# Kernel optimization log

Hardware: AMD Instinct MI355X
Metric: run time of the kernel (lower is better)

Reference implementation:

```python
import jax, jax.numpy as jnp
import numpy as np

HID = 128      # hidden_features
NF = 32        # noise_features
NPL = NF // 4  # noise features per layer
RES = 512      # noise grid resolution
N = 262144     # number of query points


def leaky_relu(x):
    return jax.nn.leaky_relu(x, negative_slope=0.01)


def sample_bilinear(image, coords):
    """image: [M, H, W]; coords: [..., M, 2] -> [..., M]"""
    M, Hn, Wn = image.shape
    x = coords[..., 0] - 0.5
    y = coords[..., 1] - 0.5
    x0f = jnp.floor(x)
    y0f = jnp.floor(y)
    xw = x - x0f
    yw = y - y0f
    x0 = x0f.astype(jnp.int32) % Wn
    x1 = (x0f.astype(jnp.int32) + 1) % Wn
    y0 = y0f.astype(jnp.int32) % Hn
    y1 = (y0f.astype(jnp.int32) + 1) % Hn
    f = jnp.arange(M)  # broadcasts against [..., M] index arrays
    i00 = image[f, y0, x0]
    i01 = image[f, y0, x1]
    i10 = image[f, y1, x0]
    i11 = image[f, y1, x1]
    i0 = i00 + (i01 - i00) * xw
    i1 = i10 + (i11 - i10) * xw
    return i0 + (i1 - i0) * yw


def setup_inputs() -> dict:
    key = jax.random.key(0)
    ks = jax.random.split(key, 12)
    noise = jax.random.normal(ks[0], (NF, RES, RES), dtype=jnp.float32)
    coords = jax.random.normal(ks[1], (N, 2), dtype=jnp.float32)
    # NoiseTransforms param: randn * 0.05 * 2**i per feature
    scale = 0.05 * (2.0 ** np.arange(NF)).astype(np.float32)
    transformations = jax.random.normal(ks[2], (NF, 2, 2), dtype=jnp.float32) * scale[:, None, None]
    input_vec = jnp.ones((HID,), dtype=jnp.float32)
    s_lin = 1.0 / np.sqrt(HID)
    s_noise = 1.0 / np.sqrt(NPL)
    lw = jax.random.uniform(ks[3], (4, HID, HID), jnp.float32, -s_lin, s_lin)
    lb = jax.random.uniform(ks[4], (4, HID), jnp.float32, -s_lin, s_lin)
    lnw = jax.random.uniform(ks[5], (4, HID, NPL), jnp.float32, -s_noise, s_noise)
    tw1 = jax.random.uniform(ks[6], (HID, HID), jnp.float32, -s_lin, s_lin)
    tb1 = jax.random.uniform(ks[7], (HID,), jnp.float32, -s_lin, s_lin)
    tw2 = jax.random.uniform(ks[8], (1, HID), jnp.float32, -s_lin, s_lin)
    tb2 = jax.random.uniform(ks[9], (1,), jnp.float32, -s_lin, s_lin)
    return {"noise": noise, "coords": coords, "transformations": transformations,
            "input_vec": input_vec, "lw": lw, "lb": lb, "lnw": lnw,
            "tw1": tw1, "tb1": tb1, "tw2": tw2, "tb2": tb2}


def reference(noise, coords, transformations, input_vec, lw, lb, lnw, tw1, tb1, tw2, tb2):
    # noise coords: [..., NF, 2]
    noise_coords = jnp.einsum('...n,Mmn->...Mm', coords, transformations)
    noise_values = sample_bilinear(noise, noise_coords)  # [..., NF]
    x = input_vec  # [HID], broadcasts up through layer adds
    for i in range(4):
        nv = noise_values[..., i * NPL:(i + 1) * NPL]
        x = leaky_relu(jnp.einsum('...h,oh->...o', x, lw[i]) + lb[i]
                       + jnp.einsum('...n,on->...o', nv, lnw[i]))
    h = leaky_relu(jnp.einsum('...h,oh->...o', x, tw1) + tb1)
    return jnp.einsum('...h,oh->...o', h, tw2) + tb2  # [..., 1]
```

## Files before the change

kernel.cpp:

```cpp
#include <hip/hip_runtime.h>

typedef _Float16 f16;
typedef f16 f16x4 __attribute__((ext_vector_type(4)));
typedef f16 f16x8 __attribute__((ext_vector_type(8)));
typedef float f32x4 __attribute__((ext_vector_type(4)));

#define RES 512
#define PTS 128
#define XS  136
#define AS  16


__device__ __forceinline__
void pack_w_body(int g, const float* __restrict__ lw, const float* __restrict__ lnw,
                 const float* __restrict__ lb, const float* __restrict__ tw1,
                 const float* __restrict__ tb1, const float* __restrict__ ivec,
                 f16* __restrict__ wf, f16* __restrict__ waugf) {
    if (g < 10240) {
        const int L = g >> 11, r = g & 2047;
        const int lane = r & 63, frag = r >> 6;
        const int q = lane >> 4, l15 = lane & 15;
        const int mt = frag >> 2, c = frag & 3;
        const float* src = ((L < 4) ? (lw + L * 16384) : tw1)
                           + (mt * 16 + l15) * 128 + c * 32 + q * 8;
        f16x8 h;
        #pragma unroll
        for (int j = 0; j < 8; ++j) h[j] = (f16)src[j];
        *(f16x8*)(wf + (size_t)g * 8) = h;
    } else {
        const int ga = g - 10240;
        const int L = ga >> 9, r = ga & 511;
        const int lane = r & 63, mt = r >> 6;
        const int q = lane >> 4, l15 = lane & 15;
        const int row = mt * 16 + l15;
        f16x8 h = {};
        if (q == 0 && L < 4) {
            const float* src = lnw + L * 1024 + row * 8;
            #pragma unroll
            for (int j = 0; j < 8; ++j) h[j] = (f16)src[j];
        }
        if (q == 1) {
            if (L == 0) {
                float s = lb[row];
                const float4* w4 = (const float4*)(lw + row * 128);
                const float4* v4 = (const float4*)ivec;
                #pragma unroll 8
                for (int k = 0; k < 32; ++k) {
                    const float4 w = w4[k], v = v4[k];
                    s += w.x * v.x + w.y * v.y + w.z * v.z + w.w * v.w;
                }
                h[0] = (f16)s;
            } else {
                h[0] = (f16)((L < 4) ? lb[L * 128 + row] : tb1[row]);
            }
        }
        *(f16x8*)(waugf + (size_t)ga * 8) = h;
    }
}

__global__ __launch_bounds__(256)
void pack_all_k(const float* __restrict__ n, f16* __restrict__ q,
                const float* __restrict__ lw,  const float* __restrict__ lnw,
                const float* __restrict__ lb,  const float* __restrict__ tw1,
                const float* __restrict__ tb1, const float* __restrict__ ivec,
                f16* __restrict__ wf, f16* __restrict__ waugf) {
    const int b = blockIdx.x;
    if (b < 8192) {
        const int idx = b * 256 + threadIdx.x;
        const int qx = idx & 255, rest = idx >> 8;
        const int qy = rest & 255, m = rest >> 8;
        const float* src = n + ((size_t)m * 512 + 2 * qy) * 512 + 2 * qx;
        const float2 r0 = *(const float2*)(src);
        const float2 r1 = *(const float2*)(src + 512);
        f16x4 o; o[0]=(f16)r0.x; o[1]=(f16)r0.y; o[2]=(f16)r1.x; o[3]=(f16)r1.y;
        *(f16x4*)(q + (size_t)idx * 4) = o;
    } else {
        pack_w_body((b - 8192) * 256 + threadIdx.x, lw, lnw, lb, tw1, tb1, ivec, wf, waugf);
    }
}

__global__ __launch_bounds__(256)
void pack_w_k(const float* __restrict__ lw,  const float* __restrict__ lnw,
              const float* __restrict__ lb,  const float* __restrict__ tw1,
              const float* __restrict__ tb1, const float* __restrict__ ivec,
              f16* __restrict__ wf, f16* __restrict__ waugf) {
    pack_w_body(blockIdx.x * 256 + threadIdx.x, lw, lnw, lb, tw1, tb1, ivec, wf, waugf);
}

__device__ __forceinline__ float quad_tap(uint2 q, int sy, int sx) {
    unsigned w = sy ? q.y : q.x;
    w >>= (sx << 4);
    union { unsigned short u; f16 h; } cv; cv.u = (unsigned short)w;
    return (float)cv.h;
}

template <bool QUAD>
__global__ __launch_bounds__(256, 4)
void sample_kernel(const void* __restrict__ noise_v,
                   const float* __restrict__ coords,
                   const float* __restrict__ trans,
                   f16* __restrict__ nv_ws, const int Ntot)
{
    __shared__ float T_sh[128];
    const int t = threadIdx.x;
    if (t < 128) T_sh[t] = trans[t];
    __syncthreads();

    const int g = blockIdx.x & 7;
    const int pb = (blockIdx.x >> 3) * 1024 + t;

    int mk[4];
    if (g < 7) { mk[0] = g; mk[1] = g + 9; mk[2] = g + 17; mk[3] = g + 25; }
    else       { mk[0] = 7; mk[1] = 8;     mk[2] = 16;     mk[3] = 24;     }

    float2 c[4];
    #pragma unroll
    for (int j = 0; j < 4; ++j)
        c[j] = *(const float2*)(coords + (pb + 256 * j) * 2);

    float nvr[4][4];
    {
        #pragma clang fp contract(off)
        #pragma unroll
        for (int j = 0; j < 4; ++j) {
            const float cx = c[j].x;
            const float cy = c[j].y;
            #pragma unroll
            for (int k = 0; k < 4; ++k) {
                const int m = mk[k];
                const float T00 = T_sh[m*4+0], T01 = T_sh[m*4+1];
                const float T10 = T_sh[m*4+2], T11 = T_sh[m*4+3];
                const float p0x = T00 * cx;
                const float p0y = T10 * cx;
                const float ncx = __builtin_fmaf(T01, cy, p0x);
                const float ncy = __builtin_fmaf(T11, cy, p0y);
                const float u = ncx - 0.5f;
                const float v = ncy - 0.5f;
                const float xf = floorf(u), yf = floorf(v);
                const float xw = u - xf, yw = v - yf;
                int ix = (xf >= 2147483648.0f || xf < -2147483648.0f) ? (int)(-2147483647 - 1) : (int)xf;
                int iy = (yf >= 2147483648.0f || yf < -2147483648.0f) ? (int)(-2147483647 - 1) : (int)yf;
                const int x0 = ix & (RES - 1);
                const int x1 = (int)(((unsigned)ix + 1u) & (unsigned)(RES - 1));
                const int y0 = iy & (RES - 1);
                const int y1 = (int)(((unsigned)iy + 1u) & (unsigned)(RES - 1));
                float i00, i01, i10, i11;
                if constexpr (QUAD) {
                    const f16* pl = (const f16*)noise_v + (size_t)m * (256 * 256 * 4);
                    const int qx0 = x0 >> 1, sx0 = x0 & 1;
                    const int qx1 = x1 >> 1, sx1 = x1 & 1;
                    const int qy0 = y0 >> 1, sy0 = y0 & 1;
                    const int qy1 = y1 >> 1, sy1 = y1 & 1;
                    const uint2 qa = *(const uint2*)(pl + (qy0 * 256 + qx0) * 4);
                    const uint2 qb = *(const uint2*)(pl + (qy0 * 256 + qx1) * 4);
                    const uint2 qc = *(const uint2*)(pl + (qy1 * 256 + qx0) * 4);
                    const uint2 qd = *(const uint2*)(pl + (qy1 * 256 + qx1) * 4);
                    i00 = quad_tap(qa, sy0, sx0);
                    i01 = quad_tap(qb, sy0, sx1);
                    i10 = quad_tap(qc, sy1, sx0);
                    i11 = quad_tap(qd, sy1, sx1);
                } else {
                    const float* pl = (const float*)noise_v + (size_t)m * (RES * RES);
                    i00 = pl[y0 * RES + x0];
                    i01 = pl[y0 * RES + x1];
                    i10 = pl[y1 * RES + x0];
                    i11 = pl[y1 * RES + x1];
                }
                const float a0 = i00 + (i01 - i00) * xw;
                const float a1 = i10 + (i11 - i10) * xw;
                nvr[j][k] = a0 + (a1 - a0) * yw;
            }
        }
    }
    #pragma unroll
    for (int j = 0; j < 4; ++j) {
        #pragma unroll
        for (int k = 0; k < 4; ++k) {
            const int m = mk[k];
            const int slot = (m & 7) * 4 + (m >> 3);
            nv_ws[(size_t)slot * Ntot + pb + 256 * j] = (f16)nvr[j][k];
        }
    }
}

__global__ __launch_bounds__(256, 2)
void mlp_kernel(const f16* __restrict__ nv_ws,
                const f16* __restrict__ wf,
                const f16* __restrict__ waugf,
                const float* __restrict__ tw2,
                const float* __restrict__ tb2,
                float* __restrict__ out, const int Ntot)
{
    __shared__ f16 Wm[16384];
    __shared__ f16 Waug[4096];
    __shared__ f16 xa[PTS * XS];
    __shared__ f16 xaug[PTS * AS];
    __shared__ __align__(16) float tw2_sh[128];

    const int t    = threadIdx.x;
    const int wave = t >> 6;
    const int lane = t & 63;
    const int q    = lane >> 4;
    const int l15  = lane & 15;
    const int pbase = blockIdx.x * PTS;
    const int pw    = wave * 32;
    const int p = t >> 1, h = t & 1;

    if (t < 128) {
        tw2_sh[t] = tw2[t];
        xaug[t * AS + 8] = (f16)1.0f;
        #pragma unroll
        for (int c = 9; c < 16; ++c) xaug[t * AS + c] = (f16)0.0f;
    }
    const float tb2_0 = tb2[0];

    f16x8 nva, nvb;
    {
        const int P = pbase + p;
        #pragma unroll
        for (int j = 0; j < 8; ++j) {
            nva[j] = nv_ws[(size_t)(j * 4 + 2 * h)     * Ntot + P];
            nvb[j] = nv_ws[(size_t)(j * 4 + 2 * h + 1) * Ntot + P];
        }
    }
    if (h == 0) *(f16x8*)&xaug[p * AS] = nva;

    {
        const f16x8 a0 = *(const f16x8*)&waugf[t * 8];
        const f16x8 a1 = *(const f16x8*)&waugf[(t + 256) * 8];
        *(f16x8*)&Waug[t * 8]         = a0;
        *(f16x8*)&Waug[(t + 256) * 8] = a1;
    }
    __syncthreads();

    const f32x4 z4 = {0.f, 0.f, 0.f, 0.f};
    f32x4 acc[2][8];
    f16x8 wreg[8], areg[2];
    #pragma unroll 1
    for (int L = 0; L < 5; ++L) {
        if (L < 4) {
            const f16* wsrc = wf + (L + 1) * 16384;
            #pragma unroll
            for (int i = 0; i < 8; ++i)
                wreg[i] = *(const f16x8*)&wsrc[(t + i * 256) * 8];
            const f16* asrc = waugf + (L + 1) * 4096;
            areg[0] = *(const f16x8*)&asrc[t * 8];
            areg[1] = *(const f16x8*)&asrc[(t + 256) * 8];
        }

        if (L == 0) {
            #pragma unroll
            for (int i = 0; i < 2; ++i)
                #pragma unroll
                for (int mt = 0; mt < 8; ++mt) acc[i][mt] = z4;
        }
        const int pr0 = (pw + l15) * XS, pr1 = (pw + 16 + l15) * XS;
        if (L) {
            #pragma unroll
            for (int c = 0; c < 4; ++c) {
                const int kc = c * 32 + q * 8;
                const f16x8 xb0 = *(const f16x8*)&xa[pr0 + kc];
                const f16x8 xb1 = *(const f16x8*)&xa[pr1 + kc];
                #pragma unroll
                for (int mt = 0; mt < 8; ++mt) {
                    const f16x8 aw = *(const f16x8*)&Wm[((mt * 4 + c) * 64 + lane) * 8];
                    const f32x4 c0 = (c == 0) ? z4 : acc[0][mt];
                    const f32x4 c1 = (c == 0) ? z4 : acc[1][mt];
                    acc[0][mt] = __builtin_amdgcn_mfma_f32_16x16x32_f16(aw, xb0, c0, 0, 0, 0);
                    acc[1][mt] = __builtin_amdgcn_mfma_f32_16x16x32_f16(aw, xb1, c1, 0, 0, 0);
                }
            }
        }
        {
            f16x8 xb0 = {}, xb1 = {};
            if (q < 2) {
                xb0 = *(const f16x8*)&xaug[(pw + l15) * AS + q * 8];
                xb1 = *(const f16x8*)&xaug[(pw + 16 + l15) * AS + q * 8];
            }
            #pragma unroll
            for (int mt = 0; mt < 8; ++mt) {
                const f16x8 aw = *(const f16x8*)&Waug[(mt * 64 + lane) * 8];
                acc[0][mt] = __builtin_amdgcn_mfma_f32_16x16x32_f16(aw, xb0, acc[0][mt], 0, 0, 0);
                acc[1][mt] = __builtin_amdgcn_mfma_f32_16x16x32_f16(aw, xb1, acc[1][mt], 0, 0, 0);
            }
        }

        if (L < 4) {
            #pragma unroll
            for (int i = 0; i < 2; ++i) {
                const int pr = (pw + i * 16 + l15) * XS;
                #pragma unroll
                for (int mt = 0; mt < 8; ++mt) {
                    f16x4 hv;
                    #pragma unroll
                    for (int r = 0; r < 4; ++r) {
                        float v = acc[i][mt][r];
                        v = fmaxf(v, 0.01f * v);
                        hv[r] = (f16)v;
                    }
                    *(f16x4*)&xa[pr + mt * 16 + q * 4] = hv;
                }
            }
            if (L < 3) {
                const int Ln = L + 1;
                if ((Ln >> 1) == h)
                    *(f16x8*)&xaug[p * AS] = (Ln & 1) ? nvb : nva;
            }
            __syncthreads();
            {
                #pragma unroll
                for (int i = 0; i < 8; ++i)
                    *(f16x8*)&Wm[(t + i * 256) * 8] = wreg[i];
                *(f16x8*)&Waug[t * 8]         = areg[0];
                *(f16x8*)&Waug[(t + 256) * 8] = areg[1];
            }
            __syncthreads();
        } else {
            #pragma unroll
            for (int i = 0; i < 2; ++i) {
                float s = 0.f;
                #pragma unroll
                for (int mt = 0; mt < 8; ++mt) {
                    const f32x4 w4 = *(const f32x4*)&tw2_sh[mt * 16 + q * 4];
                    #pragma unroll
                    for (int r = 0; r < 4; ++r) {
                        float v = acc[i][mt][r];
                        v = fmaxf(v, 0.01f * v);
                        s += w4[r] * v;
                    }
                }
                s += __shfl_xor(s, 16);
                s += __shfl_xor(s, 32);
                if (q == 0) out[pbase + pw + i * 16 + l15] = s + tb2_0;
            }
        }
    }
}

extern "C" void kernel_launch(void* const* d_in, const int* in_sizes, int n_in,
                              void* d_out, int out_size, void* d_ws, size_t ws_size,
                              hipStream_t stream) {
    const float* noise  = (const float*)d_in[0];
    const float* coords = (const float*)d_in[1];
    const float* trans  = (const float*)d_in[2];
    const float* ivec   = (const float*)d_in[3];
    const float* lw     = (const float*)d_in[4];
    const float* lb     = (const float*)d_in[5];
    const float* lnw    = (const float*)d_in[6];
    const float* tw1    = (const float*)d_in[7];
    const float* tb1    = (const float*)d_in[8];
    const float* tw2    = (const float*)d_in[9];
    const float* tb2    = (const float*)d_in[10];
    float* o            = (float*)d_out;

    const int N = in_sizes[1] / 2;
    f16* nv    = (f16*)d_ws;
    const size_t NV = (size_t)N * 32;
    f16* wfp   = nv + NV;
    f16* waugp = wfp + 5 * 16384;
    f16* qn    = waugp + 5 * 4096;
    const size_t need_full = (NV + 5 * 16384 + 5 * 4096
                              + (size_t)32 * 256 * 256 * 4) * sizeof(f16);

    if (ws_size >= need_full) {
        pack_all_k<<<8192 + 50, 256, 0, stream>>>(noise, qn, lw, lnw, lb, tw1, tb1,
                                                  ivec, wfp, waugp);
        sample_kernel<true><<<(N / 1024) * 8, 256, 0, stream>>>(qn, coords, trans, nv, N);
    } else {
        pack_w_k<<<50, 256, 0, stream>>>(lw, lnw, lb, tw1, tb1, ivec, wfp, waugp);
        sample_kernel<false><<<(N / 1024) * 8, 256, 0, stream>>>(noise, coords, trans, nv, N);
    }
    mlp_kernel<<<N / PTS, 256, 0, stream>>>(nv, wfp, waugp, tw2, tb2, o, N);
}
```

Before: 207.0 us.

## Retile MLP MFMA work as 2x2 wave grid over points and outputs

Changes the wave decomposition from each wave owning 32 points and all 128 outputs to a 2x2 grid where each wave owns 64 points and 64 outputs. Each weight fragment loaded from LDS is now reused across four point groups instead of two, cutting LDS weight reads per MFMA. The cost is that x-activation reads double per wave, and the final projection needs a cross-wave reduction through shared memory plus an extra barrier.

Result: no change. 205.7 us (-0.6%).

```diff
diff --git a/kernel.cpp b/kernel.cpp
--- a/kernel.cpp
+++ b/kernel.cpp
@@ -196,14 +196,16 @@
     __shared__ f16 xa[PTS * XS];
     __shared__ f16 xaug[PTS * AS];
     __shared__ __align__(16) float tw2_sh[128];
+    __shared__ float pp[2][PTS];
 
     const int t    = threadIdx.x;
     const int wave = t >> 6;
     const int lane = t & 63;
     const int q    = lane >> 4;
     const int l15  = lane & 15;
+    const int wi   = wave >> 1;
+    const int wj   = wave & 1;
     const int pbase = blockIdx.x * PTS;
-    const int pw    = wave * 32;
     const int p = t >> 1, h = t & 1;
 
     if (t < 128) {
@@ -234,7 +236,7 @@
     __syncthreads();
 
     const f32x4 z4 = {0.f, 0.f, 0.f, 0.f};
-    f32x4 acc[2][8];
+    f32x4 acc[4][4];
     f16x8 wreg[8], areg[2];
     #pragma unroll 1
     for (int L = 0; L < 5; ++L) {
@@ -250,55 +252,60 @@
 
         if (L == 0) {
             #pragma unroll
-            for (int i = 0; i < 2; ++i)
-                #pragma unroll
-                for (int mt = 0; mt < 8; ++mt) acc[i][mt] = z4;
-        }
-        const int pr0 = (pw + l15) * XS, pr1 = (pw + 16 + l15) * XS;
+            for (int pg = 0; pg < 4; ++pg)
+                #pragma unroll
+                for (int mtl = 0; mtl < 4; ++mtl) acc[pg][mtl] = z4;
+        }
         if (L) {
             #pragma unroll
             for (int c = 0; c < 4; ++c) {
                 const int kc = c * 32 + q * 8;
-                const f16x8 xb0 = *(const f16x8*)&xa[pr0 + kc];
-                const f16x8 xb1 = *(const f16x8*)&xa[pr1 + kc];
-                #pragma unroll
-                for (int mt = 0; mt < 8; ++mt) {
-                    const f16x8 aw = *(const f16x8*)&Wm[((mt * 4 + c) * 64 + lane) * 8];
-                    const f32x4 c0 = (c == 0) ? z4 : acc[0][mt];
-                    const f32x4 c1 = (c == 0) ? z4 : acc[1][mt];
-                    acc[0][mt] = __builtin_amdgcn_mfma_f32_16x16x32_f16(aw, xb0, c0, 0, 0, 0);
-                    acc[1][mt] = __builtin_amdgcn_mfma_f32_16x16x32_f16(aw, xb1, c1, 0, 0, 0);
+                f16x8 xb[4];
+                #pragma unroll
+                for (int pg = 0; pg < 4; ++pg)
+                    xb[pg] = *(const f16x8*)&xa[(wi * 64 + pg * 16 + l15) * XS + kc];
+                #pragma unroll
+                for (int mtl = 0; mtl < 4; ++mtl) {
+                    const f16x8 aw = *(const f16x8*)
+                        &Wm[(((wj * 4 + mtl) * 4 + c) * 64 + lane) * 8];
+                    #pragma unroll
+                    for (int pg = 0; pg < 4; ++pg) {
+                        const f32x4 ci = (c == 0) ? z4 : acc[pg][mtl];
+                        acc[pg][mtl] = __builtin_amdgcn_mfma_f32_16x16x32_f16(aw, xb[pg], ci, 0, 0, 0);
+                    }
                 }
             }
         }
         {
-            f16x8 xb0 = {}, xb1 = {};
+            f16x8 xb[4] = {};
             if (q < 2) {
-                xb0 = *(const f16x8*)&xaug[(pw + l15) * AS + q * 8];
-                xb1 = *(const f16x8*)&xaug[(pw + 16 + l15) * AS + q * 8];
-            }
-            #pragma unroll
-            for (int mt = 0; mt < 8; ++mt) {
-                const f16x8 aw = *(const f16x8*)&Waug[(mt * 64 + lane) * 8];
-                acc[0][mt] = __builtin_amdgcn_mfma_f32_16x16x32_f16(aw, xb0, acc[0][mt], 0, 0, 0);
-                acc[1][mt] = __builtin_amdgcn_mfma_f32_16x16x32_f16(aw, xb1, acc[1][mt], 0, 0, 0);
+                #pragma unroll
+                for (int pg = 0; pg < 4; ++pg)
+                    xb[pg] = *(const f16x8*)&xaug[(wi * 64 + pg * 16 + l15) * AS + q * 8];
+            }
+            #pragma unroll
+            for (int mtl = 0; mtl < 4; ++mtl) {
+                const f16x8 aw = *(const f16x8*)&Waug[((wj * 4 + mtl) * 64 + lane) * 8];
+                #pragma unroll
+                for (int pg = 0; pg < 4; ++pg)
+                    acc[pg][mtl] = __builtin_amdgcn_mfma_f32_16x16x32_f16(aw, xb[pg], acc[pg][mtl], 0, 0, 0);
             }
         }
 
         if (L < 4) {
             #pragma unroll
-            for (int i = 0; i < 2; ++i) {
-                const int pr = (pw + i * 16 + l15) * XS;
-                #pragma unroll
-                for (int mt = 0; mt < 8; ++mt) {
+            for (int pg = 0; pg < 4; ++pg) {
+                const int pr = (wi * 64 + pg * 16 + l15) * XS;
+                #pragma unroll
+                for (int mtl = 0; mtl < 4; ++mtl) {
                     f16x4 hv;
                     #pragma unroll
                     for (int r = 0; r < 4; ++r) {
-                        float v = acc[i][mt][r];
+                        float v = acc[pg][mtl][r];
                         v = fmaxf(v, 0.01f * v);
                         hv[r] = (f16)v;
                     }
-                    *(f16x4*)&xa[pr + mt * 16 + q * 4] = hv;
+                    *(f16x4*)&xa[pr + wj * 64 + mtl * 16 + q * 4] = hv;
                 }
             }
             if (L < 3) {
@@ -317,22 +324,25 @@
             __syncthreads();
         } else {
             #pragma unroll
-            for (int i = 0; i < 2; ++i) {
+            for (int pg = 0; pg < 4; ++pg) {
                 float s = 0.f;
                 #pragma unroll
-                for (int mt = 0; mt < 8; ++mt) {
-                    const f32x4 w4 = *(const f32x4*)&tw2_sh[mt * 16 + q * 4];
+                for (int mtl = 0; mtl < 4; ++mtl) {
+                    const f32x4 w4 = *(const f32x4*)&tw2_sh[wj * 64 + mtl * 16 + q * 4];
                     #pragma unroll
                     for (int r = 0; r < 4; ++r) {
-                        float v = acc[i][mt][r];
+                        float v = acc[pg][mtl][r];
                         v = fmaxf(v, 0.01f * v);
                         s += w4[r] * v;
                     }
                 }
                 s += __shfl_xor(s, 16);
                 s += __shfl_xor(s, 32);
-                if (q == 0) out[pbase + pw + i * 16 + l15] = s + tb2_0;
-            }
+                if (q == 0) pp[wj][wi * 64 + pg * 16 + l15] = s;
+            }
+            __syncthreads();
+            if (t < 128)
+                out[pbase + t] = pp[0][t] + pp[1][t] + tb2_0;
         }
     }
 }
```
